# Kernel tuning notes

Measured on AMD Instinct MI355X. Metric: run time of the kernel, lower is better.

## Reference

```python
import jax, jax.numpy as jnp
import numpy as np

S, B, E = 1024, 2, 1024   # seq, batch, emsize
H = 16                    # nheads
HD = E // H               # head dim
D_FF = 4096               # nhid
N_EXP = 8                 # num experts (world_size=1 -> all local)
EPS = 1e-5


def setup_inputs() -> dict:
    key = jax.random.key(0)
    ks = jax.random.split(key, 12)
    s = 0.02
    return {
        "x": jax.random.normal(ks[0], (S, B, E), jnp.float32),
        "in_proj_w": jax.random.normal(ks[1], (3 * E, E), jnp.float32) * s,
        "in_proj_b": jnp.zeros((3 * E,), jnp.float32),
        "out_proj_w": jax.random.normal(ks[2], (E, E), jnp.float32) * s,
        "out_proj_b": jnp.zeros((E,), jnp.float32),
        "ln1_g": jnp.ones((E,), jnp.float32),
        "ln1_b": jnp.zeros((E,), jnp.float32),
        "ln2_g": jnp.ones((E,), jnp.float32),
        "ln2_b": jnp.zeros((E,), jnp.float32),
        "gate_w": jax.random.normal(ks[3], (N_EXP, E), jnp.float32) * s,
        "gate_b": jnp.zeros((N_EXP,), jnp.float32),
        "w1": jax.random.normal(ks[4], (N_EXP, D_FF, E), jnp.float32) * s,
        "b1": jnp.zeros((N_EXP, D_FF), jnp.float32),
        "w2": jax.random.normal(ks[5], (N_EXP, E, D_FF), jnp.float32) * s,
        "b2": jnp.zeros((N_EXP, E), jnp.float32),
    }


def _layernorm(x, g, b):
    mu = jnp.mean(x, axis=-1, keepdims=True)
    var = jnp.var(x, axis=-1, keepdims=True)
    return (x - mu) * jax.lax.rsqrt(var + EPS) * g + b


def _mha(x, in_proj_w, in_proj_b, out_proj_w, out_proj_b):
    # x: [S, B, E] (torch MultiheadAttention default layout)
    qkv = x @ in_proj_w.T + in_proj_b                # [S, B, 3E]
    q, k, v = jnp.split(qkv, 3, axis=-1)
    q = q.reshape(S, B, H, HD) * (1.0 / np.sqrt(HD))
    k = k.reshape(S, B, H, HD)
    v = v.reshape(S, B, H, HD)
    scores = jnp.einsum("sbhd,tbhd->bhst", q, k)     # [B, H, S, S]
    attn = jax.nn.softmax(scores, axis=-1)
    o = jnp.einsum("bhst,tbhd->sbhd", attn, v).reshape(S, B, E)
    return o @ out_proj_w.T + out_proj_b


def _moe(x, gate_w, gate_b, w1, b1, w2, b2):
    # top-1 routing (fmoe NaiveGate, top_k=1 -> combine weight is exactly 1.0)
    t = x.reshape(S * B, E)
    logits = t @ gate_w.T + gate_b                   # [T, N_EXP]
    eid = jnp.argmax(logits, axis=-1)                # [T]
    out = jnp.zeros_like(t)
    for e in range(N_EXP):                           # fixed small expert loop
        h = jax.nn.gelu(t @ w1[e].T + b1[e], approximate=False) @ w2[e].T + b2[e]
        out = out + jnp.where((eid == e)[:, None], h, 0.0)
    return out.reshape(S, B, E)


def reference(x, in_proj_w, in_proj_b, out_proj_w, out_proj_b,
              ln1_g, ln1_b, ln2_g, ln2_b,
              gate_w, gate_b, w1, b1, w2, b2):
    x = _layernorm(x + _mha(x, in_proj_w, in_proj_b, out_proj_w, out_proj_b), ln1_g, ln1_b)
    x = _layernorm(x + _moe(x, gate_w, gate_b, w1, b1, w2, b2), ln2_g, ln2_b)
    return x
```

## Files before the change

### kernel.cpp

```cpp
#include <hip/hip_runtime.h>
#include <hip/hip_bf16.h>
#include <math.h>

#define DI __device__ __forceinline__

typedef __bf16 bf16_t;
typedef bf16_t bf16x8 __attribute__((ext_vector_type(8)));
typedef bf16_t bf16x4 __attribute__((ext_vector_type(4)));
typedef float f32x4 __attribute__((ext_vector_type(4)));

constexpr int S_ = 1024, B_ = 2, E_ = 1024, H_ = 16, HD_ = 64;
constexpr int T_ = S_ * B_;
constexpr int DFF_ = 4096, NE_ = 8;
constexpr int SLOTS_ = 3072;
constexpr int SPLITK_ = 4;

DI f32x4 mfma16(bf16x8 a, bf16x8 b, f32x4 c) {
  return __builtin_amdgcn_mfma_f32_16x16x32_bf16(a, b, c, 0, 0, 0);
}

DI void split2(float v, bf16_t& h, bf16_t& l) {
  h = (bf16_t)v;
  l = (bf16_t)(v - (float)h);
}

typedef const __attribute__((address_space(1))) void* gas_p;
typedef __attribute__((address_space(3))) void* las_p;
DI void gll16(const void* g, void* l) {
  __builtin_amdgcn_global_load_lds((gas_p)g, (las_p)l, 16, 0, 0);
}

DI int swslot(int u, int r) { return u ^ (r & 7); }

template <int NCH, int LOG2NCH>
DI void prep_w_load(const float* src, int f, f32x4& a, f32x4& b) {
  int u = f & 7, chunk = (f >> 3) & (NCH - 1), row = f >> (3 + LOG2NCH);
  const float* s = src + (size_t)row * (NCH * 64) + chunk * 64 + u * 8;
  a = *(const f32x4*)s;
  b = *(const f32x4*)(s + 4);
}
template <int NCH, int LOG2NCH>
DI void prep_w_store(bf16_t* dst, int f, f32x4 a, f32x4 b) {
  int u = f & 7, chunk = (f >> 3) & (NCH - 1), row = f >> (3 + LOG2NCH);
  bf16x8 o;
#pragma unroll
  for (int j = 0; j < 4; j++) { o[j] = (bf16_t)a[j]; o[4 + j] = (bf16_t)b[j]; }
  char* d = (char*)dst + (size_t)row * (NCH * 128) + chunk * 128 + swslot(u, row) * 16;
  *(bf16x8*)d = o;
}

DI void do_prep_wsplit(const float* src, bf16_t* dst, int f) {
  int u = f & 3, chunk = (f >> 2) & 31, row = f >> 7;
  const float* s = src + (size_t)row * 1024 + chunk * 32 + u * 8;
  f32x4 a = *(const f32x4*)s, b = *(const f32x4*)(s + 4);
  bf16x8 hv, lv;
#pragma unroll
  for (int j = 0; j < 4; j++) {
    bf16_t h, l; split2(a[j], h, l); hv[j] = h; lv[j] = l;
    split2(b[j], h, l); hv[4 + j] = h; lv[4 + j] = l;
  }
  char* base = (char*)dst + (size_t)row * 4096 + chunk * 128;
  *(bf16x8*)(base + swslot(u, row) * 16) = hv;
  *(bf16x8*)(base + swslot(u + 4, row) * 16) = lv;
}

__launch_bounds__(256)
__global__ void prep_all(const float* ipw, bf16_t* ipwp,
                         const float* opw, bf16_t* opwp,
                         const float* x, bf16_t* xp, int* cnt) {
  int b = blockIdx.x, tid = threadIdx.x;
  if (b < 1536) {
    do_prep_wsplit(ipw, ipwp, b * 256 + tid);
  } else if (b < 2048) {
    do_prep_wsplit(opw, opwp, (b - 1536) * 256 + tid);
  } else if (b < 3072) {
    do_prep_wsplit(x, xp, (b - 2048) * 256 + tid);
  } else {
    if (tid < 8) cnt[tid] = 0;
  }
}

template <int MODE>
__launch_bounds__(256, 2)
__global__ void gemm_kernel(const bf16_t* Ap, const bf16_t* Bp0,
                            const float* bias,
                            float* Cf, bf16_t* Cb,
                            bf16_t* Qh, bf16_t* Ql, bf16_t* Kh2, bf16_t* Kl2,
                            bf16_t* Vh2, bf16_t* Vl2,
                            const int* offs_pad,
                            const float* W1f, bf16_t* W1p,
                            const float* W2f, bf16_t* W2p) {
  constexpr bool SPLIT = (MODE <= 1);
  constexpr int NK = (MODE == 0) ? 32 : 16;
  constexpr int ARB = (MODE == 2) ? 2048 : ((MODE == 3) ? 8192 : 4096);
  constexpr int BUFB = 32768;
  extern __shared__ char smem[];

  const int tid = threadIdx.x, lane = tid & 63, wv = tid >> 6;
  int n0, m0;
  if constexpr (MODE == 0) {
    int b = blockIdx.x;
    if (b >= 384) {
      int bu = (b - 384) * 8;
      f32x4 va[8], vb[8];
      if (bu < 16384) {
#pragma unroll
        for (int it = 0; it < 8; it++)
          prep_w_load<16, 4>(W1f, (bu + it) * 256 + tid, va[it], vb[it]);
#pragma unroll
        for (int it = 0; it < 8; it++)
          prep_w_store<16, 4>(W1p, (bu + it) * 256 + tid, va[it], vb[it]);
      } else {
        int b2 = bu - 16384;
#pragma unroll
        for (int it = 0; it < 8; it++)
          prep_w_load<64, 6>(W2f, (b2 + it) * 256 + tid, va[it], vb[it]);
#pragma unroll
        for (int it = 0; it < 8; it++)
          prep_w_store<64, 6>(W2p, (b2 + it) * 256 + tid, va[it], vb[it]);
      }
      return;
    }
    n0 = (b % 24) * 128;
    m0 = (b / 24) * 128;
  } else {
    n0 = blockIdx.x * 128;
    m0 = blockIdx.y * 128;
  }

  int e = 0;
  if constexpr (MODE >= 2) {
    if (m0 >= offs_pad[8]) return;
#pragma unroll
    for (int i = 1; i < 8; i++) e += (m0 >= offs_pad[i]);
  }
  const int kz = (MODE == 1 || MODE == 3) ? blockIdx.z : 0;
  const int ck0 = (MODE == 1 || MODE == 3) ? kz * 16 : 0;

  const char* Ab = (const char*)Ap;
  const char* Bb = (const char*)Bp0;
  if constexpr (MODE == 2) Bb += (size_t)e * 4096 * 2048;
  if constexpr (MODE == 3) Bb += (size_t)e * 1024 * 8192;

  auto STAGE = [&](char* lb, int ck) {
#pragma unroll
    for (int i = 0; i < 4; i++) {
      int f = i * 256 + tid, row = f >> 3, cb = (f & 7) * 16;
      gll16(Ab + (size_t)(m0 + row) * ARB + ck * 128 + cb, lb + f * 16);
    }
#pragma unroll
    for (int i = 0; i < 4; i++) {
      int f = i * 256 + tid, row = f >> 3, cb = (f & 7) * 16;
      gll16(Bb + (size_t)(n0 + row) * ARB + ck * 128 + cb, lb + 16384 + f * 16);
    }
  };

  f32x4 acc[4][4];
#pragma unroll
  for (int i = 0; i < 4; i++)
#pragma unroll
    for (int j = 0; j < 4; j++) acc[i][j] = (f32x4){0.f, 0.f, 0.f, 0.f};

  const int wm = (wv >> 1) * 64, wn = (wv & 1) * 64;
  const int lr = lane & 15;

  auto LB = [&](const char* base, int r, int u) {
    return *(const bf16x8*)(base + r * 128 + (swslot(u, r) << 4));
  };
  auto COMPUTE = [&](const char* lb) {
    const char* Abase = lb;
    const char* Bbase = lb + 16384;
    if constexpr (SPLIT) {
      const int u = lane >> 4;
      bf16x8 afh[4], afl[4];
#pragma unroll
      for (int fm = 0; fm < 4; fm++) {
        int r = wm + fm * 16 + lr;
        afh[fm] = LB(Abase, r, u);
        afl[fm] = LB(Abase, r, u + 4);
      }
#pragma unroll
      for (int fn = 0; fn < 4; fn++) {
        int r = wn + fn * 16 + lr;
        bf16x8 bfh = LB(Bbase, r, u);
        bf16x8 bfl = LB(Bbase, r, u + 4);
#pragma unroll
        for (int fm = 0; fm < 4; fm++) {
          acc[fm][fn] = mfma16(afh[fm], bfh, acc[fm][fn]);
          acc[fm][fn] = mfma16(afh[fm], bfl, acc[fm][fn]);
          acc[fm][fn] = mfma16(afl[fm], bfh, acc[fm][fn]);
        }
      }
    } else {
#pragma unroll
      for (int kk = 0; kk < 2; kk++) {
        const int u = kk * 4 + (lane >> 4);
        bf16x8 af[4];
#pragma unroll
        for (int fm = 0; fm < 4; fm++) af[fm] = LB(Abase, wm + fm * 16 + lr, u);
#pragma unroll
        for (int fn = 0; fn < 4; fn++) {
          bf16x8 bf = LB(Bbase, wn + fn * 16 + lr, u);
#pragma unroll
          for (int fm = 0; fm < 4; fm++) acc[fm][fn] = mfma16(af[fm], bf, acc[fm][fn]);
        }
      }
    }
  };

  STAGE(smem, ck0);
  __syncthreads();
  int cur = 0;
  for (int kt = 0; kt < NK; ++kt) {
    if (kt + 1 < NK) STAGE(smem + (cur ^ 1) * BUFB, ck0 + kt + 1);
    COMPUTE(smem + cur * BUFB);
    __syncthreads();
    cur ^= 1;
  }

  const int lr4 = (lane >> 4) * 4;
#pragma unroll
  for (int fm = 0; fm < 4; fm++) {
#pragma unroll
    for (int fn = 0; fn < 4; fn++) {
#pragma unroll
      for (int r = 0; r < 4; r++) {
        float v = acc[fm][fn][r];
        int row = wm + fm * 16 + lr4 + r;
        int col = wn + fn * 16 + lr;
        if constexpr (MODE == 0) {
          int gm = m0 + row, gn = n0 + col;
          v += bias[gn];
          int sec = gn >> 10, ee = gn & 1023, hh = ee >> 6, dd = ee & 63;
          if (sec == 0) v *= 0.125f;
          int ss = gm >> 1, bb = gm & 1, bhp = bb * 16 + hh;
          size_t base = ((size_t)bhp * 1024 + ss) * 64;
          bf16_t oh, ol; split2(v, oh, ol);
          if (sec == 0) {
            Qh[base + dd] = oh; Ql[base + dd] = ol;
          } else {
            size_t di = base + ((size_t)swslot(dd >> 3, ss) << 3) + (dd & 7);
            bf16_t* dh = (sec == 1) ? Kh2 : Vh2;
            bf16_t* dl = (sec == 1) ? Kl2 : Vl2;
            dh[di] = oh; dl[di] = ol;
          }
        } else if constexpr (MODE == 1) {
          int gm = m0 + row, gn = n0 + col;
          Cf[((size_t)kz * T_ + gm) * E_ + gn] = v;
        } else if constexpr (MODE == 2) {
          int slot = m0 + row, gn = n0 + col;
          v += bias[e * DFF_ + gn];
          v = 0.5f * v * (1.0f + erff(v * 0.70710678118654752440f));
          size_t byte = (size_t)slot * 8192 + (gn >> 6) * 128 +
                        (swslot((gn & 63) >> 3, slot) << 4) + (gn & 7) * 2;
          *(bf16_t*)((char*)Cb + byte) = (bf16_t)v;
        } else {
          int slot = m0 + row, gn = n0 + col;
          Cb[((size_t)kz * SLOTS_ + slot) * E_ + gn] = (bf16_t)v;
        }
      }
    }
  }
}

__launch_bounds__(256)
__global__ void vtrans_kernel(const bf16_t* vh, const bf16_t* vl,
                              bf16_t* vth, bf16_t* vtl) {
  const int bh = blockIdx.y, s0 = blockIdx.x * 64;
  const int tid = threadIdx.x;
  __shared__ bf16_t th[64][72];
  __shared__ bf16_t tl[64][72];
#pragma unroll
  for (int i = 0; i < 2; i++) {
    int f = tid + i * 256, r = f >> 3, c = (f & 7) * 8;
    int s = s0 + r;
    size_t rowb = ((size_t)bh * 1024 + s) * 128;
    *(bf16x8*)&th[r][c] = *(const bf16x8*)((const char*)vh + rowb + (swslot(c >> 3, s) << 4));
    *(bf16x8*)&tl[r][c] = *(const bf16x8*)((const char*)vl + rowb + (swslot(c >> 3, s) << 4));
  }
  __syncthreads();
#pragma unroll
  for (int i = 0; i < 2; i++) {
    int f = tid + i * 256, d = f >> 3, c2 = (f & 7) * 8;
    bf16x8 oh, ol;
#pragma unroll
    for (int j = 0; j < 8; j++) { oh[j] = th[c2 + j][d]; ol[j] = tl[c2 + j][d]; }
    size_t ob = (((size_t)bh * 64 + d) * 1024 + s0) * 2;
    *(bf16x8*)((char*)vth + ob + (swslot(c2 >> 3, d) << 4)) = oh;
    *(bf16x8*)((char*)vtl + ob + (swslot(c2 >> 3, d) << 4)) = ol;
  }
}

__launch_bounds__(256)
__global__ void attn_kernel(const bf16_t* gqh, const bf16_t* gql,
                            const bf16_t* gkh, const bf16_t* gkl,
                            const bf16_t* gvth, const bf16_t* gvtl,
                            bf16_t* ao) {
  const int bh = blockIdx.y, q0 = blockIdx.x * 64;
  const int tid = threadIdx.x, lane = tid & 63, wv = tid >> 6;
  const int lr = lane & 15, lk = (lane >> 4) * 8, lr4 = (lane >> 4) * 4;
  extern __shared__ char smem[];
  char* Kh = smem;
  char* Kl = smem + 8192;
  char* Vh = smem + 16384;
  char* Vl = smem + 24576;
  char* Ph = smem + 32768;
  char* Pl = smem + 40960;

  const size_t qbase = ((size_t)bh * 1024 + q0 + wv * 16 + lr) * 64;
  bf16x8 qfh[2], qfl[2];
  qfh[0] = *(const bf16x8*)&gqh[qbase + lk];
  qfh[1] = *(const bf16x8*)&gqh[qbase + 32 + lk];
  qfl[0] = *(const bf16x8*)&gql[qbase + lk];
  qfl[1] = *(const bf16x8*)&gql[qbase + 32 + lk];

  f32x4 oacc[4];
#pragma unroll
  for (int i = 0; i < 4; i++) oacc[i] = (f32x4){0.f, 0.f, 0.f, 0.f};
  float m_r[4], l_r[4];
#pragma unroll
  for (int r = 0; r < 4; r++) { m_r[r] = -INFINITY; l_r[r] = 0.f; }

  for (int t0 = 0; t0 < S_; t0 += 64) {
    __syncthreads();
#pragma unroll
    for (int i = 0; i < 2; i++) {
      int f = i * 256 + tid, row = f >> 3, cb = (f & 7) * 16;
      size_t koff = ((size_t)bh * 1024 + t0 + row) * 128 + cb;
      gll16((const char*)gkh + koff, Kh + f * 16);
      gll16((const char*)gkl + koff, Kl + f * 16);
      size_t voff = (((size_t)bh * 64 + row) * 1024 + t0) * 2 + cb;
      gll16((const char*)gvth + voff, Vh + f * 16);
      gll16((const char*)gvtl + voff, Vl + f * 16);
    }
    __syncthreads();

    f32x4 sacc[4];
#pragma unroll
    for (int i = 0; i < 4; i++) sacc[i] = (f32x4){0.f, 0.f, 0.f, 0.f};
#pragma unroll
    for (int kk = 0; kk < 2; ++kk) {
      const int u = kk * 4 + (lane >> 4);
#pragma unroll
      for (int fn = 0; fn < 4; ++fn) {
        int r = fn * 16 + lr;
        bf16x8 kbh = *(const bf16x8*)(Kh + r * 128 + (swslot(u, r) << 4));
        bf16x8 kbl = *(const bf16x8*)(Kl + r * 128 + (swslot(u, r) << 4));
        sacc[fn] = mfma16(qfh[kk], kbh, sacc[fn]);
        sacc[fn] = mfma16(qfh[kk], kbl, sacc[fn]);
        sacc[fn] = mfma16(qfl[kk], kbh, sacc[fn]);
      }
    }
#pragma unroll
    for (int r = 0; r < 4; r++) {
      float mx = fmaxf(fmaxf(sacc[0][r], sacc[1][r]), fmaxf(sacc[2][r], sacc[3][r]));
#pragma unroll
      for (int off = 1; off < 16; off <<= 1) mx = fmaxf(mx, __shfl_xor(mx, off));
      float mn = m_r[r];
      if (mx > mn) {
        mn = mx;
        float al = __expf(m_r[r] - mn);
        l_r[r] *= al;
#pragma unroll
        for (int fd = 0; fd < 4; fd++) oacc[fd][r] *= al;
        m_r[r] = mn;
      }
      float ps = 0.f;
      int pr = wv * 16 + lr4 + r;
#pragma unroll
      for (int fn = 0; fn < 4; fn++) {
        float p = __expf(sacc[fn][r] - mn);
        ps += p;
        bf16_t ph, pl; split2(p, ph, pl);
        int colu = (fn * 16 + lr) >> 3;
        int byte = pr * 128 + (swslot(colu, pr) << 4) + ((lr & 7) * 2);
        *(bf16_t*)(Ph + byte) = ph;
        *(bf16_t*)(Pl + byte) = pl;
      }
#pragma unroll
      for (int off = 1; off < 16; off <<= 1) ps += __shfl_xor(ps, off);
      l_r[r] += ps;
    }
#pragma unroll
    for (int kk = 0; kk < 2; kk++) {
      const int u = kk * 4 + (lane >> 4);
      int pr2 = wv * 16 + lr;
      bf16x8 pah = *(const bf16x8*)(Ph + pr2 * 128 + (swslot(u, pr2) << 4));
      bf16x8 pal = *(const bf16x8*)(Pl + pr2 * 128 + (swslot(u, pr2) << 4));
#pragma unroll
      for (int fd = 0; fd < 4; fd++) {
        int rd = fd * 16 + lr;
        bf16x8 vbh = *(const bf16x8*)(Vh + rd * 128 + (swslot(u, rd) << 4));
        bf16x8 vbl = *(const bf16x8*)(Vl + rd * 128 + (swslot(u, rd) << 4));
        oacc[fd] = mfma16(pah, vbh, oacc[fd]);
        oacc[fd] = mfma16(pah, vbl, oacc[fd]);
        oacc[fd] = mfma16(pal, vbh, oacc[fd]);
      }
    }
  }
  const int b = bh >> 4, h = bh & 15;
#pragma unroll
  for (int fd = 0; fd < 4; fd++) {
#pragma unroll
    for (int r = 0; r < 4; r++) {
      float v = oacc[fd][r] / l_r[r];
      int s = q0 + wv * 16 + lr4 + r;
      int d = fd * 16 + lr;
      int tok = s * 2 + b;
      int chunk = h * 2 + (d >> 5);
      int w = d & 31;
      bf16_t oh, ol; split2(v, oh, ol);
      size_t rb = (size_t)tok * 4096 + chunk * 128;
      *(bf16_t*)((char*)ao + rb + (swslot(w >> 3, tok) << 4) + (w & 7) * 2) = oh;
      *(bf16_t*)((char*)ao + rb + (swslot(4 + (w >> 3), tok) << 4) + (w & 7) * 2) = ol;
    }
  }
}

__launch_bounds__(256)
__global__ void ln1gate_kernel(const float* p0, const float* p1, const float* x,
                               const float* opb, const float* g, const float* bt,
                               const float* gw, const float* gb,
                               float* l1f, int* eid, int* cnt) {
  const int row = blockIdx.x, tid = threadIdx.x;
  const int j = tid * 4;
  f32x4 v = *(const f32x4*)&p0[(size_t)row * 1024 + j];
  f32x4 v1 = *(const f32x4*)&p1[(size_t)row * 1024 + j];
  f32x4 xr = *(const f32x4*)&x[(size_t)row * 1024 + j];
  f32x4 bb2 = *(const f32x4*)&opb[j];
#pragma unroll
  for (int i = 0; i < 4; i++) v[i] += v1[i] + xr[i] + bb2[i];
  float s = v[0] + v[1] + v[2] + v[3];
  float q = v[0] * v[0] + v[1] * v[1] + v[2] * v[2] + v[3] * v[3];
#pragma unroll
  for (int off = 1; off < 64; off <<= 1) { s += __shfl_xor(s, off); q += __shfl_xor(q, off); }
  __shared__ float ss[4], qq[4];
  __shared__ float gp[4][8];
  int wv = tid >> 6;
  if ((tid & 63) == 0) { ss[wv] = s; qq[wv] = q; }
  __syncthreads();
  s = ss[0] + ss[1] + ss[2] + ss[3];
  q = qq[0] + qq[1] + qq[2] + qq[3];
  float mu = s * (1.f / 1024.f);
  float var = q * (1.f / 1024.f) - mu * mu;
  float rs = rsqrtf(var + 1e-5f);
  f32x4 gg = *(const f32x4*)&g[j];
  f32x4 bb = *(const f32x4*)&bt[j];
  f32x4 o;
#pragma unroll
  for (int jj = 0; jj < 4; jj++) o[jj] = (v[jj] - mu) * rs * gg[jj] + bb[jj];
  *(f32x4*)&l1f[(size_t)row * 1024 + j] = o;

  float a[8];
#pragma unroll
  for (int ee = 0; ee < 8; ee++) {
    f32x4 wv4 = *(const f32x4*)&gw[ee * 1024 + j];
    a[ee] = o[0] * wv4[0] + o[1] * wv4[1] + o[2] * wv4[2] + o[3] * wv4[3];
  }
#pragma unroll
  for (int ee = 0; ee < 8; ee++)
#pragma unroll
    for (int off = 1; off < 64; off <<= 1) a[ee] += __shfl_xor(a[ee], off);
  if ((tid & 63) == 0) {
#pragma unroll
    for (int ee = 0; ee < 8; ee++) gp[wv][ee] = a[ee];
  }
  __syncthreads();
  if (tid == 0) {
    float best = -1e30f;
    int be = 0;
#pragma unroll
    for (int ee = 0; ee < 8; ee++) {
      float vv = gp[0][ee] + gp[1][ee] + gp[2][ee] + gp[3][ee] + gb[ee];
      if (vv > best) { best = vv; be = ee; }
    }
    eid[row] = be;
    atomicAdd(&cnt[be], 1);
  }
}

__launch_bounds__(256)
__global__ void ln2_kernel(const bf16_t* part, const float* l1f, const float* b2,
                           const int* eid, const int* inv, const float* g,
                           const float* bt, float* out) {
  const int t = blockIdx.x, tid = threadIdx.x;
  const int st = inv[t], e = eid[t];
  const int j = tid * 4;
  f32x4 v = (f32x4){0.f, 0.f, 0.f, 0.f};
#pragma unroll
  for (int kz = 0; kz < SPLITK_; kz++) {
    bf16x4 p = *(const bf16x4*)&part[((size_t)kz * SLOTS_ + st) * 1024 + j];
#pragma unroll
    for (int i = 0; i < 4; i++) v[i] += (float)p[i];
  }
  f32x4 bb2 = *(const f32x4*)&b2[e * 1024 + j];
  f32x4 rr = *(const f32x4*)&l1f[(size_t)t * 1024 + j];
#pragma unroll
  for (int i = 0; i < 4; i++) v[i] += bb2[i] + rr[i];
  float s = v[0] + v[1] + v[2] + v[3];
  float q = v[0] * v[0] + v[1] * v[1] + v[2] * v[2] + v[3] * v[3];
#pragma unroll
  for (int off = 1; off < 64; off <<= 1) { s += __shfl_xor(s, off); q += __shfl_xor(q, off); }
  __shared__ float ss[4], qq[4];
  int wv = tid >> 6;
  if ((tid & 63) == 0) { ss[wv] = s; qq[wv] = q; }
  __syncthreads();
  s = ss[0] + ss[1] + ss[2] + ss[3];
  q = qq[0] + qq[1] + qq[2] + qq[3];
  float mu = s * (1.f / 1024.f);
  float var = q * (1.f / 1024.f) - mu * mu;
  float rs = rsqrtf(var + 1e-5f);
  f32x4 gg = *(const f32x4*)&g[j];
  f32x4 bb = *(const f32x4*)&bt[j];
  f32x4 o;
#pragma unroll
  for (int jj = 0; jj < 4; jj++) o[jj] = (v[jj] - mu) * rs * gg[jj] + bb[jj];
  *(f32x4*)&out[(size_t)t * 1024 + j] = o;
}

__global__ void scan_kernel(const int* cnt, int* offs_pad, int* cur) {
  if (threadIdx.x == 0) {
    int op = 0;
    for (int e = 0; e < 8; e++) {
      offs_pad[e] = op;
      op += (cnt[e] + 127) & ~127;
      cur[e] = 0;
    }
    offs_pad[8] = op;
  }
}

__launch_bounds__(256)
__global__ void scatter_gather(const int* eid, const int* offs_pad, int* cur,
                               int* inv, const float* l1f, bf16_t* l1g) {
  const int t = blockIdx.x * 4 + (threadIdx.x >> 6);
  const int lane = threadIdx.x & 63;
  int slot = 0;
  if (lane == 0) {
    int ee = eid[t];
    int pos = atomicAdd(&cur[ee], 1);
    slot = offs_pad[ee] + pos;
    inv[t] = slot;
  }
  slot = __shfl(slot, 0);
#pragma unroll
  for (int i = 0; i < 2; i++) {
    int chunk = (lane >> 3) + i * 8, u = lane & 7;
    const float* s = l1f + (size_t)t * 1024 + chunk * 64 + u * 8;
    f32x4 a = *(const f32x4*)s, b = *(const f32x4*)(s + 4);
    bf16x8 o;
#pragma unroll
    for (int j = 0; j < 4; j++) { o[j] = (bf16_t)a[j]; o[4 + j] = (bf16_t)b[j]; }
    char* d = (char*)l1g + (size_t)slot * 2048 + chunk * 128 + swslot(u, slot) * 16;
    *(bf16x8*)d = o;
  }
}

extern "C" void kernel_launch(void* const* d_in, const int* in_sizes, int n_in,
                              void* d_out, int out_size, void* d_ws, size_t ws_size,
                              hipStream_t stream) {
  const float* x    = (const float*)d_in[0];
  const float* ipw  = (const float*)d_in[1];
  const float* ipb  = (const float*)d_in[2];
  const float* opw  = (const float*)d_in[3];
  const float* opb  = (const float*)d_in[4];
  const float* ln1g = (const float*)d_in[5];
  const float* ln1b = (const float*)d_in[6];
  const float* ln2g = (const float*)d_in[7];
  const float* ln2b = (const float*)d_in[8];
  const float* gw   = (const float*)d_in[9];
  const float* gb   = (const float*)d_in[10];
  const float* w1   = (const float*)d_in[11];
  const float* b1   = (const float*)d_in[12];
  const float* w2   = (const float*)d_in[13];
  const float* b2   = (const float*)d_in[14];
  float* out = (float*)d_out;

  char* w = (char*)d_ws;
  auto alloc = [&](size_t n) { char* p = w; w += (n + 255) & ~(size_t)255; return p; };
  const size_t MB = 1u << 20;

  char* R1 = alloc(64 * MB);
  bf16_t* w1p   = (bf16_t*)R1;
  bf16_t* partb = (bf16_t*)R1;
  bf16_t* w2p = (bf16_t*)alloc(64 * MB);
  char* R3 = alloc(8 * MB);
  bf16_t* xp  = (bf16_t*)R3;
  bf16_t* l1g = (bf16_t*)R3;
  bf16_t* ipwp = (bf16_t*)alloc(12 * MB);
  bf16_t* opwp = (bf16_t*)alloc(4 * MB);
  char* R6 = alloc(32 * MB);
  bf16_t* qh  = (bf16_t*)(R6 + 0 * MB);
  bf16_t* ql  = (bf16_t*)(R6 + 4 * MB);
  bf16_t* kh  = (bf16_t*)(R6 + 8 * MB);
  bf16_t* kl  = (bf16_t*)(R6 + 12 * MB);
  bf16_t* vh  = (bf16_t*)(R6 + 16 * MB);
  bf16_t* vl  = (bf16_t*)(R6 + 20 * MB);
  bf16_t* vth = (bf16_t*)(R6 + 24 * MB);
  bf16_t* vtl = (bf16_t*)(R6 + 28 * MB);
  bf16_t* hbuf = (bf16_t*)R6;
  bf16_t* ao    = (bf16_t*)alloc(8 * MB);
  float*  pre1p = (float*)alloc(16 * MB);
  float*  l1f   = (float*)alloc(8 * MB);
  int* eid   = (int*)alloc(T_ * 4);
  int* cnt   = (int*)alloc(16 * 4);
  int* offsp = (int*)alloc(16 * 4);
  int* cur   = (int*)alloc(16 * 4);
  int* inv   = (int*)alloc(T_ * 4);

  const dim3 blk(256);
  const int smemGemm = 65536;
  const int smemAttn = 49152;

  prep_all<<<dim3(3073), blk, 0, stream>>>(ipw, ipwp, opw, opwp, x, xp, cnt);

  gemm_kernel<0><<<dim3(4480), blk, smemGemm, stream>>>(
      xp, ipwp, ipb, nullptr, nullptr,
      qh, ql, kh, kl, vh, vl, nullptr,
      w1, w1p, w2, w2p);

  vtrans_kernel<<<dim3(16, 32), blk, 0, stream>>>(vh, vl, vth, vtl);

  attn_kernel<<<dim3(16, 32), blk, smemAttn, stream>>>(qh, ql, kh, kl, vth, vtl, ao);

  gemm_kernel<1><<<dim3(8, 16, 2), blk, smemGemm, stream>>>(
      ao, opwp, nullptr, pre1p, nullptr,
      nullptr, nullptr, nullptr, nullptr, nullptr, nullptr, nullptr,
      nullptr, nullptr, nullptr, nullptr);

  ln1gate_kernel<<<dim3(T_), blk, 0, stream>>>(pre1p, pre1p + (size_t)T_ * E_, x,
                                               opb, ln1g, ln1b, gw, gb,
                                               l1f, eid, cnt);

  scan_kernel<<<1, 64, 0, stream>>>(cnt, offsp, cur);
  scatter_gather<<<dim3(T_ / 4), blk, 0, stream>>>(eid, offsp, cur, inv, l1f, l1g);

  gemm_kernel<2><<<dim3(32, 24, 1), blk, smemGemm, stream>>>(
      l1g, w1p, b1, nullptr, hbuf,
      nullptr, nullptr, nullptr, nullptr, nullptr, nullptr, offsp,
      nullptr, nullptr, nullptr, nullptr);

  gemm_kernel<3><<<dim3(8, 24, SPLITK_), blk, smemGemm, stream>>>(
      hbuf, w2p, nullptr, nullptr, partb,
      nullptr, nullptr, nullptr, nullptr, nullptr, nullptr, offsp,
      nullptr, nullptr, nullptr, nullptr);

  ln2_kernel<<<dim3(T_), blk, 0, stream>>>(partb, l1f, b2, eid, inv, ln2g, ln2b, out);

  (void)in_sizes; (void)n_in; (void)out_size; (void)ws_size;
}
```

Before: 358.3 us.

## Redistribute expert weight bf16 conversion across attention and FFN1 kernels

Moves the W1 fp32-to-bf16 split conversion out of the QKV GEMM launch and into extra blocks of the attention kernel. The W2 conversion moves into extra blocks of the expert FFN1 GEMM. The goal is to overlap weight-conversion memory traffic with kernels that have idle CU capacity, and to shorten the QKV GEMM launch. It requires 1D block indexing in attention and FFN1, and risks that the conversion blocks contend with the compute blocks in those kernels.

Result: faster. 334.2 us (-6.7%).

```diff
diff --git a/kernel.cpp b/kernel.cpp
--- a/kernel.cpp
+++ b/kernel.cpp
@@ -88,7 +88,6 @@
                             bf16_t* Qh, bf16_t* Ql, bf16_t* Kh2, bf16_t* Kl2,
                             bf16_t* Vh2, bf16_t* Vl2,
                             const int* offs_pad,
-                            const float* W1f, bf16_t* W1p,
                             const float* W2f, bf16_t* W2p) {
   constexpr bool SPLIT = (MODE <= 1);
   constexpr int NK = (MODE == 0) ? 32 : 16;
@@ -98,31 +97,21 @@
 
   const int tid = threadIdx.x, lane = tid & 63, wv = tid >> 6;
   int n0, m0;
-  if constexpr (MODE == 0) {
+  if constexpr (MODE == 2) {
     int b = blockIdx.x;
-    if (b >= 384) {
-      int bu = (b - 384) * 8;
+    if (b >= 768) {
+      int bu = (b - 768) * 8;
       f32x4 va[8], vb[8];
-      if (bu < 16384) {
-#pragma unroll
-        for (int it = 0; it < 8; it++)
-          prep_w_load<16, 4>(W1f, (bu + it) * 256 + tid, va[it], vb[it]);
-#pragma unroll
-        for (int it = 0; it < 8; it++)
-          prep_w_store<16, 4>(W1p, (bu + it) * 256 + tid, va[it], vb[it]);
-      } else {
-        int b2 = bu - 16384;
-#pragma unroll
-        for (int it = 0; it < 8; it++)
-          prep_w_load<64, 6>(W2f, (b2 + it) * 256 + tid, va[it], vb[it]);
-#pragma unroll
-        for (int it = 0; it < 8; it++)
-          prep_w_store<64, 6>(W2p, (b2 + it) * 256 + tid, va[it], vb[it]);
-      }
+#pragma unroll
+      for (int it = 0; it < 8; it++)
+        prep_w_load<64, 6>(W2f, (bu + it) * 256 + tid, va[it], vb[it]);
+#pragma unroll
+      for (int it = 0; it < 8; it++)
+        prep_w_store<64, 6>(W2p, (bu + it) * 256 + tid, va[it], vb[it]);
       return;
     }
-    n0 = (b % 24) * 128;
-    m0 = (b / 24) * 128;
+    n0 = (b & 31) * 128;
+    m0 = (b >> 5) * 128;
   } else {
     n0 = blockIdx.x * 128;
     m0 = blockIdx.y * 128;
@@ -295,9 +284,24 @@
 __global__ void attn_kernel(const bf16_t* gqh, const bf16_t* gql,
                             const bf16_t* gkh, const bf16_t* gkl,
                             const bf16_t* gvth, const bf16_t* gvtl,
-                            bf16_t* ao) {
-  const int bh = blockIdx.y, q0 = blockIdx.x * 64;
+                            bf16_t* ao,
+                            const float* W1f, bf16_t* W1p) {
   const int tid = threadIdx.x, lane = tid & 63, wv = tid >> 6;
+  {
+    int b = blockIdx.x;
+    if (b >= 512) {
+      int bu = (b - 512) * 8;
+      f32x4 va[8], vb[8];
+#pragma unroll
+      for (int it = 0; it < 8; it++)
+        prep_w_load<16, 4>(W1f, (bu + it) * 256 + tid, va[it], vb[it]);
+#pragma unroll
+      for (int it = 0; it < 8; it++)
+        prep_w_store<16, 4>(W1p, (bu + it) * 256 + tid, va[it], vb[it]);
+      return;
+    }
+  }
+  const int bh = blockIdx.x >> 4, q0 = (blockIdx.x & 15) * 64;
   const int lr = lane & 15, lk = (lane >> 4) * 8, lr4 = (lane >> 4) * 4;
   extern __shared__ char smem[];
   char* Kh = smem;
@@ -614,19 +618,19 @@
 
   prep_all<<<dim3(3073), blk, 0, stream>>>(ipw, ipwp, opw, opwp, x, xp, cnt);
 
-  gemm_kernel<0><<<dim3(4480), blk, smemGemm, stream>>>(
+  gemm_kernel<0><<<dim3(24, 16), blk, smemGemm, stream>>>(
       xp, ipwp, ipb, nullptr, nullptr,
-      qh, ql, kh, kl, vh, vl, nullptr,
-      w1, w1p, w2, w2p);
+      qh, ql, kh, kl, vh, vl, nullptr, nullptr, nullptr);
 
   vtrans_kernel<<<dim3(16, 32), blk, 0, stream>>>(vh, vl, vth, vtl);
 
-  attn_kernel<<<dim3(16, 32), blk, smemAttn, stream>>>(qh, ql, kh, kl, vth, vtl, ao);
+  attn_kernel<<<dim3(2560), blk, smemAttn, stream>>>(qh, ql, kh, kl, vth, vtl,
+                                                     ao, w1, w1p);
 
   gemm_kernel<1><<<dim3(8, 16, 2), blk, smemGemm, stream>>>(
       ao, opwp, nullptr, pre1p, nullptr,
       nullptr, nullptr, nullptr, nullptr, nullptr, nullptr, nullptr,
-      nullptr, nullptr, nullptr, nullptr);
+      nullptr, nullptr);
 
   ln1gate_kernel<<<dim3(T_), blk, 0, stream>>>(pre1p, pre1p + (size_t)T_ * E_, x,
                                                opb, ln1g, ln1b, gw, gb,
@@ -635,15 +639,15 @@
   scan_kernel<<<1, 64, 0, stream>>>(cnt, offsp, cur);
   scatter_gather<<<dim3(T_ / 4), blk, 0, stream>>>(eid, offsp, cur, inv, l1f, l1g);
 
-  gemm_kernel<2><<<dim3(32, 24, 1), blk, smemGemm, stream>>>(
+  gemm_kernel<2><<<dim3(2816), blk, smemGemm, stream>>>(
       l1g, w1p, b1, nullptr, hbuf,
       nullptr, nullptr, nullptr, nullptr, nullptr, nullptr, offsp,
-      nullptr, nullptr, nullptr, nullptr);
+      w2, w2p);
 
   gemm_kernel<3><<<dim3(8, 24, SPLITK_), blk, smemGemm, stream>>>(
       hbuf, w2p, nullptr, nullptr, partb,
       nullptr, nullptr, nullptr, nullptr, nullptr, nullptr, offsp,
-      nullptr, nullptr, nullptr, nullptr);
+      nullptr, nullptr);
 
   ln2_kernel<<<dim3(T_), blk, 0, stream>>>(partb, l1f, b2, eid, inv, ln2g, ln2b, out);
 
```
